# Performance work log

Measured on AMD Instinct MI355X. Metric: run time of the kernel, lower is better.

The kernel has to match this reference:

```python
import jax, jax.numpy as jnp
import numpy as np

B, N, C = 8, 1024, 1024
H = 16
D = C // H  # head_dim = 64
SCALE = D ** -0.5


def setup_inputs() -> dict:
    key = jax.random.key(0)
    k1, k2, k3 = jax.random.split(key, 3)
    x = jax.random.normal(k1, (B, N, C), dtype=jnp.float32)
    w_qkv = jax.random.normal(k2, (3 * C, C), dtype=jnp.float32) * (C ** -0.5)
    w_proj = jax.random.normal(k3, (C, C), dtype=jnp.float32) * (C ** -0.5)
    b_proj = jnp.zeros((C,), dtype=jnp.float32)
    return {"x": x, "w_qkv": w_qkv, "w_proj": w_proj, "b_proj": b_proj}


def reference(x, w_qkv, w_proj, b_proj):
    Bx, Nx, Cx = x.shape
    # qkv: [B,N,3C] -> [3,B,H,N,D]
    qkv = jnp.einsum('bnc,oc->bno', x, w_qkv)
    qkv = qkv.reshape(Bx, Nx, 3, H, D).transpose(2, 0, 3, 1, 4)
    q, k, v = qkv[0], qkv[1], qkv[2]
    attn = jnp.einsum('bhnd,bhmd->bhnm', q, k) * SCALE  # [B,H,N,N]
    attn = jax.nn.softmax(attn, axis=-1)
    out = jnp.einsum('bhnm,bhmd->bhnd', attn, v)  # [B,H,N,D]
    out = out.transpose(0, 2, 1, 3).reshape(Bx, Nx, Cx)
    return jnp.einsum('bnc,oc->bno', out, w_proj) + b_proj
```

## Files before the change

kernel.cpp:

```cpp
#include <hip/hip_runtime.h>

typedef _Float16 half8 __attribute__((ext_vector_type(8)));
typedef _Float16 half4v __attribute__((ext_vector_type(4)));
typedef _Float16 half2v __attribute__((ext_vector_type(2)));
typedef float floatx4 __attribute__((ext_vector_type(4)));

#define AS3 __attribute__((address_space(3)))
#define AS1 __attribute__((address_space(1)))

__global__ __launch_bounds__(256) void cvt_all(const float* __restrict__ x,
                                               const float* __restrict__ wq,
                                               const float* __restrict__ wp,
                                               _Float16* __restrict__ xh,
                                               _Float16* __restrict__ wqh,
                                               _Float16* __restrict__ wph) {
    long i = (long)blockIdx.x * 256 + threadIdx.x;
    const float4* src; half4v* dst; long off;
    if (i < 2097152)      { src = (const float4*)x;  dst = (half4v*)xh;  off = i; }
    else if (i < 2883584) { src = (const float4*)wq; dst = (half4v*)wqh; off = i - 2097152; }
    else                  { src = (const float4*)wp; dst = (half4v*)wph; off = i - 2883584; }
    float4 v = src[off];
    half4v h = {(_Float16)v.x, (_Float16)v.y, (_Float16)v.z, (_Float16)v.w};
    dst[off] = h;
}

__global__ __launch_bounds__(256, 4) void gemm_tn(
    const _Float16* __restrict__ A, const _Float16* __restrict__ B,
    _Float16* __restrict__ Ch, int ldc, _Float16* __restrict__ Vt, int split,
    float* __restrict__ Cf, const float* __restrict__ bias,
    int M, int Nn, int K)
{
    __shared__ _Float16 sA[2][128 * 32];
    __shared__ _Float16 sB[2][128 * 32];
    const int tid  = threadIdx.x;
    const int lane = tid & 63, wave = tid >> 6;
    const int quad = lane >> 4, l16 = lane & 15;
    const int wr = wave >> 1, wc = wave & 1;
    const long m0 = (long)blockIdx.x * 128, n0 = (long)blockIdx.y * 128;

    const int srow = tid >> 2;
    const int sslot = ((tid & 3) ^ ((srow >> 1) & 3)) * 8;
    const int dlo = srow * 32 + sslot;
    const int dhi = (srow + 64) * 32 + sslot;
    const _Float16* gA0 = A + (m0 + srow) * (long)K + (tid & 3) * 8;
    const _Float16* gA1 = A + (m0 + srow + 64) * (long)K + (tid & 3) * 8;
    const _Float16* gB0 = B + (n0 + srow) * (long)K + (tid & 3) * 8;
    const _Float16* gB1 = B + (n0 + srow + 64) * (long)K + (tid & 3) * 8;

    const int swz = (l16 >> 1) & 3;
    const int aoff = ((quad ^ swz) * 8);

    floatx4 acc[4][4] = {};
    const int nk = K >> 5;

    half8 rA0 = *(const half8*)gA0, rA1 = *(const half8*)gA1;
    half8 rB0 = *(const half8*)gB0, rB1 = *(const half8*)gB1;
    *(half8*)&sA[0][dlo] = rA0; *(half8*)&sA[0][dhi] = rA1;
    *(half8*)&sB[0][dlo] = rB0; *(half8*)&sB[0][dhi] = rB1;

    for (int kk = 0; kk < nk; kk++) {
        const int cur = kk & 1;
        __syncthreads();
        const bool more = (kk + 1 < nk);
        if (more) {
            const long k0 = (long)(kk + 1) << 5;
            rA0 = *(const half8*)(gA0 + k0); rA1 = *(const half8*)(gA1 + k0);
            rB0 = *(const half8*)(gB0 + k0); rB1 = *(const half8*)(gB1 + k0);
        }

        const _Float16* cA = &sA[cur][0];
        const _Float16* cB = &sB[cur][0];
        half8 af[4], bf[4];
#pragma unroll
        for (int t = 0; t < 4; t++)
            af[t] = *(const half8*)&cA[(wr * 64 + t * 16 + l16) * 32 + aoff];
#pragma unroll
        for (int t = 0; t < 4; t++)
            bf[t] = *(const half8*)&cB[(wc * 64 + t * 16 + l16) * 32 + aoff];
#pragma unroll
        for (int tm = 0; tm < 4; tm++)
#pragma unroll
            for (int tn = 0; tn < 4; tn++)
                acc[tm][tn] = __builtin_amdgcn_mfma_f32_16x16x32_f16(af[tm], bf[tn], acc[tm][tn], 0, 0, 0);

        if (more) {
            _Float16* nA = &sA[cur ^ 1][0];
            _Float16* nB = &sB[cur ^ 1][0];
            *(half8*)&nA[dlo] = rA0; *(half8*)&nA[dhi] = rA1;
            *(half8*)&nB[dlo] = rB0; *(half8*)&nB[dhi] = rB1;
        }
    }

#pragma unroll
    for (int tm = 0; tm < 4; tm++) {
        long row = m0 + wr * 64 + tm * 16 + quad * 4;
#pragma unroll
        for (int tn = 0; tn < 4; tn++) {
            long col = n0 + wc * 64 + tn * 16 + l16;
            if (Cf) {
                float bv = bias ? bias[col] : 0.f;
#pragma unroll
                for (int r = 0; r < 4; r++)
                    Cf[(row + r) * (long)Nn + col] = acc[tm][tn][r] + bv;
            } else if (col >= split) {
                long cv = col - split;
                long vrow = ((row >> 10) * 16 + (cv >> 6)) * 64 + (cv & 63);
                long nn = row & 1023;
                half4v pv = {(_Float16)acc[tm][tn][0], (_Float16)acc[tm][tn][1],
                             (_Float16)acc[tm][tn][2], (_Float16)acc[tm][tn][3]};
                *(half4v*)&Vt[vrow * 1024 + nn] = pv;
            } else {
#pragma unroll
                for (int r = 0; r < 4; r++)
                    Ch[(row + r) * (long)ldc + col] = (_Float16)acc[tm][tn][r];
            }
        }
    }
}

#define QSC 0.18033688f
__global__ __launch_bounds__(256, 3) void flash_attn(const _Float16* __restrict__ qk,
                                                     const _Float16* __restrict__ vt,
                                                     _Float16* __restrict__ out)
{
    const int bh = blockIdx.x, b = bh >> 4, h = bh & 15;
    const int n0 = blockIdx.y * 128;
    const int tid = threadIdx.x, lane = tid & 63, wave = tid >> 6;
    const int quad = lane >> 4, l16 = lane & 15;

    __shared__ _Float16 sK[64 * 72];
    __shared__ _Float16 sVT[64 * 72];
    __shared__ _Float16 sPT[4][32 * 72];

    half8 qf[2][2];
    const _Float16 qs = (_Float16)QSC;
    const _Float16* qbase = qk + (long)(b * 1024 + n0 + wave * 32) * 2048 + h * 64;
#pragma unroll
    for (int t = 0; t < 2; t++)
#pragma unroll
        for (int s = 0; s < 2; s++) {
            half8 v = *(const half8*)(qbase + (long)(t * 16 + l16) * 2048 + s * 32 + quad * 8);
#pragma unroll
            for (int j = 0; j < 8; j++) v[j] *= qs;
            qf[t][s] = v;
        }

    const int srow = tid >> 3, scol8 = (tid & 7) * 8;
    const _Float16* kgb = qk + 1024 + h * 64 + scol8 + (long)(b * 1024 + srow) * 2048;
    const _Float16* vgb = vt + (long)(bh * 64 + srow) * 1024 + scol8;

    float m_[2] = {-1e30f, -1e30f}, l_[2] = {0.f, 0.f};
    floatx4 o[2][4] = {};

    half8 kreg[2], vreg[2];
#pragma unroll
    for (int i = 0; i < 2; i++) {
        kreg[i] = *(const half8*)(kgb + (long)(i * 32) * 2048);
        vreg[i] = *(const half8*)(vgb + (long)(i * 32) * 1024);
    }

    for (int kt = 0; kt < 16; kt++) {
        __syncthreads();
#pragma unroll
        for (int i = 0; i < 2; i++) {
            *(half8*)&sK[(srow + i * 32) * 72 + scol8]  = kreg[i];
            *(half8*)&sVT[(srow + i * 32) * 72 + scol8] = vreg[i];
        }
        __syncthreads();
        if (kt + 1 < 16) {
            const int kr1 = (kt + 1) * 64;
#pragma unroll
            for (int i = 0; i < 2; i++) {
                kreg[i] = *(const half8*)(kgb + (long)(kr1 + i * 32) * 2048);
                vreg[i] = *(const half8*)(vgb + (long)(i * 32) * 1024 + kr1);
            }
        }

        floatx4 sacc[2][4] = {};
#pragma unroll
        for (int c = 0; c < 4; c++)
#pragma unroll
            for (int s = 0; s < 2; s++) {
                half8 kf = *(const half8*)&sK[(c * 16 + l16) * 72 + s * 32 + quad * 8];
                sacc[0][c] = __builtin_amdgcn_mfma_f32_16x16x32_f16(kf, qf[0][s], sacc[0][c], 0, 0, 0);
                sacc[1][c] = __builtin_amdgcn_mfma_f32_16x16x32_f16(kf, qf[1][s], sacc[1][c], 0, 0, 0);
            }

#pragma unroll
        for (int t = 0; t < 2; t++) {
            float mx = -1e30f;
#pragma unroll
            for (int c = 0; c < 4; c++)
#pragma unroll
                for (int r = 0; r < 4; r++) mx = fmaxf(mx, sacc[t][c][r]);
            mx = fmaxf(mx, __shfl_xor(mx, 16));
            mx = fmaxf(mx, __shfl_xor(mx, 32));
            float mn = fmaxf(m_[t], mx);
            float al = exp2f(m_[t] - mn);
            m_[t] = mn;
            float rs = 0.f;
#pragma unroll
            for (int c = 0; c < 4; c++)
#pragma unroll
                for (int r = 0; r < 4; r++) {
                    float p = exp2f(sacc[t][c][r] - mn);
                    sacc[t][c][r] = p;
                    rs += p;
                }
            rs += __shfl_xor(rs, 16);
            rs += __shfl_xor(rs, 32);
            l_[t] = l_[t] * al + rs;
#pragma unroll
            for (int dt = 0; dt < 4; dt++) o[t][dt] *= al;
#pragma unroll
            for (int c = 0; c < 4; c++) {
                half4v p = {(_Float16)sacc[t][c][0], (_Float16)sacc[t][c][1],
                            (_Float16)sacc[t][c][2], (_Float16)sacc[t][c][3]};
                *(half4v*)&sPT[wave][(t * 16 + l16) * 72 + c * 16 + quad * 4] = p;
            }
        }

#pragma unroll
        for (int kk = 0; kk < 2; kk++) {
            half8 pf0 = *(const half8*)&sPT[wave][(l16) * 72 + kk * 32 + quad * 8];
            half8 pf1 = *(const half8*)&sPT[wave][(16 + l16) * 72 + kk * 32 + quad * 8];
#pragma unroll
            for (int dt = 0; dt < 4; dt++) {
                half8 vf = *(const half8*)&sVT[(dt * 16 + l16) * 72 + kk * 32 + quad * 8];
                o[0][dt] = __builtin_amdgcn_mfma_f32_16x16x32_f16(vf, pf0, o[0][dt], 0, 0, 0);
                o[1][dt] = __builtin_amdgcn_mfma_f32_16x16x32_f16(vf, pf1, o[1][dt], 0, 0, 0);
            }
        }
    }

#pragma unroll
    for (int t = 0; t < 2; t++) {
        float inv = 1.f / l_[t];
#pragma unroll
        for (int dt = 0; dt < 4; dt++) {
            floatx4 v = o[t][dt];
            half4v a = {(_Float16)(v[0] * inv), (_Float16)(v[1] * inv),
                        (_Float16)(v[2] * inv), (_Float16)(v[3] * inv)};
            *(half4v*)&sPT[wave][(t * 16 + l16) * 72 + dt * 16 + quad * 4] = a;
        }
    }
    __syncthreads();
#pragma unroll
    for (int i = 0; i < 4; i++) {
        int ql = i * 8 + (lane >> 3);
        int c8 = (lane & 7) * 8;
        half8 vv = *(const half8*)&sPT[wave][ql * 72 + c8];
        *(half8*)(out + (long)(b * 1024 + n0 + wave * 32 + ql) * 1024 + h * 64 + c8) = vv;
    }
}

extern "C" void kernel_launch(void* const* d_in, const int* in_sizes, int n_in,
                              void* d_out, int out_size, void* d_ws, size_t ws_size,
                              hipStream_t stream) {
    const float* x      = (const float*)d_in[0];
    const float* w_qkv  = (const float*)d_in[1];
    const float* w_proj = (const float*)d_in[2];
    const float* b_proj = (const float*)d_in[3];

    char* ws = (char*)d_ws;
    _Float16* qkh    = (_Float16*)ws;
    _Float16* vT     = (_Float16*)(ws + 33554432);
    _Float16* xh     = (_Float16*)(ws + 50331648);
    _Float16* wqkvh  = (_Float16*)(ws + 67108864);
    _Float16* wprojh = (_Float16*)(ws + 73400320);
    _Float16* attnh  = xh;

    cvt_all<<<12288, 256, 0, stream>>>(x, w_qkv, w_proj, xh, wqkvh, wprojh);

    gemm_tn<<<dim3(64, 24), 256, 0, stream>>>(xh, wqkvh, qkh, 2048, vT, 2048,
                                              nullptr, nullptr, 8192, 3072, 1024);
    flash_attn<<<dim3(128, 8), 256, 0, stream>>>(qkh, vT, attnh);
    gemm_tn<<<dim3(64, 8), 256, 0, stream>>>(attnh, wprojh, nullptr, 0, nullptr, 1 << 30,
                                             (float*)d_out, b_proj, 8192, 1024, 1024);
}
```

Measured before the change: 261.9 us.

## Deepen GEMM global prefetch to two stages, drop attention register prefetch, retune occupancy

```diff
diff --git a/kernel.cpp b/kernel.cpp
--- a/kernel.cpp
+++ b/kernel.cpp
@@ -2,7 +2,6 @@
 
 typedef _Float16 half8 __attribute__((ext_vector_type(8)));
 typedef _Float16 half4v __attribute__((ext_vector_type(4)));
-typedef _Float16 half2v __attribute__((ext_vector_type(2)));
 typedef float floatx4 __attribute__((ext_vector_type(4)));
 
 #define AS3 __attribute__((address_space(3)))
@@ -24,7 +23,7 @@
     dst[off] = h;
 }
 
-__global__ __launch_bounds__(256, 4) void gemm_tn(
+__global__ __launch_bounds__(256, 3) void gemm_tn(
     const _Float16* __restrict__ A, const _Float16* __restrict__ B,
     _Float16* __restrict__ Ch, int ldc, _Float16* __restrict__ Vt, int split,
     float* __restrict__ Cf, const float* __restrict__ bias,
@@ -53,41 +52,52 @@
     floatx4 acc[4][4] = {};
     const int nk = K >> 5;
 
-    half8 rA0 = *(const half8*)gA0, rA1 = *(const half8*)gA1;
-    half8 rB0 = *(const half8*)gB0, rB1 = *(const half8*)gB1;
-    *(half8*)&sA[0][dlo] = rA0; *(half8*)&sA[0][dhi] = rA1;
-    *(half8*)&sB[0][dlo] = rB0; *(half8*)&sB[0][dhi] = rB1;
-
-    for (int kk = 0; kk < nk; kk++) {
-        const int cur = kk & 1;
-        __syncthreads();
-        const bool more = (kk + 1 < nk);
-        if (more) {
-            const long k0 = (long)(kk + 1) << 5;
-            rA0 = *(const half8*)(gA0 + k0); rA1 = *(const half8*)(gA1 + k0);
-            rB0 = *(const half8*)(gB0 + k0); rB1 = *(const half8*)(gB1 + k0);
-        }
-
-        const _Float16* cA = &sA[cur][0];
-        const _Float16* cB = &sB[cur][0];
-        half8 af[4], bf[4];
-#pragma unroll
-        for (int t = 0; t < 4; t++)
-            af[t] = *(const half8*)&cA[(wr * 64 + t * 16 + l16) * 32 + aoff];
-#pragma unroll
-        for (int t = 0; t < 4; t++)
-            bf[t] = *(const half8*)&cB[(wc * 64 + t * 16 + l16) * 32 + aoff];
-#pragma unroll
-        for (int tm = 0; tm < 4; tm++)
-#pragma unroll
-            for (int tn = 0; tn < 4; tn++)
-                acc[tm][tn] = __builtin_amdgcn_mfma_f32_16x16x32_f16(af[tm], bf[tn], acc[tm][tn], 0, 0, 0);
-
-        if (more) {
-            _Float16* nA = &sA[cur ^ 1][0];
-            _Float16* nB = &sB[cur ^ 1][0];
-            *(half8*)&nA[dlo] = rA0; *(half8*)&nA[dhi] = rA1;
-            *(half8*)&nB[dlo] = rB0; *(half8*)&nB[dhi] = rB1;
+    {
+        half8 a0 = *(const half8*)gA0, a1 = *(const half8*)gA1;
+        half8 b0 = *(const half8*)gB0, b1 = *(const half8*)gB1;
+        *(half8*)&sA[0][dlo] = a0; *(half8*)&sA[0][dhi] = a1;
+        *(half8*)&sB[0][dlo] = b0; *(half8*)&sB[0][dhi] = b1;
+    }
+    half8 pA0[2], pA1[2], pB0[2], pB1[2];
+    pA0[0] = *(const half8*)(gA0 + 32); pA1[0] = *(const half8*)(gA1 + 32);
+    pB0[0] = *(const half8*)(gB0 + 32); pB1[0] = *(const half8*)(gB1 + 32);
+
+    for (int kk = 0; kk < nk; kk += 2) {
+#pragma unroll
+        for (int u = 0; u < 2; u++) {
+            const int k = kk + u;
+            __syncthreads();
+            if (k + 2 < nk) {
+                const long ko = (long)(k + 2) << 5;
+                pA0[u ^ 1] = *(const half8*)(gA0 + ko);
+                pA1[u ^ 1] = *(const half8*)(gA1 + ko);
+                pB0[u ^ 1] = *(const half8*)(gB0 + ko);
+                pB1[u ^ 1] = *(const half8*)(gB1 + ko);
+            }
+
+            const _Float16* cA = &sA[u][0];
+            const _Float16* cB = &sB[u][0];
+            half8 af[4], bf[4];
+#pragma unroll
+            for (int t = 0; t < 4; t++)
+                af[t] = *(const half8*)&cA[(wr * 64 + t * 16 + l16) * 32 + aoff];
+#pragma unroll
+            for (int t = 0; t < 4; t++)
+                bf[t] = *(const half8*)&cB[(wc * 64 + t * 16 + l16) * 32 + aoff];
+#pragma unroll
+            for (int tm = 0; tm < 4; tm++)
+#pragma unroll
+                for (int tn = 0; tn < 4; tn++)
+                    acc[tm][tn] = __builtin_amdgcn_mfma_f32_16x16x32_f16(af[tm], bf[tn], acc[tm][tn], 0, 0, 0);
+
+            if (k + 1 < nk) {
+                _Float16* nA = &sA[u ^ 1][0];
+                _Float16* nB = &sB[u ^ 1][0];
+                *(half8*)&nA[dlo] = pA0[u];
+                *(half8*)&nA[dhi] = pA1[u];
+                *(half8*)&nB[dlo] = pB0[u];
+                *(half8*)&nB[dhi] = pB1[u];
+            }
         }
     }
 
@@ -119,7 +129,7 @@
 }
 
 #define QSC 0.18033688f
-__global__ __launch_bounds__(256, 3) void flash_attn(const _Float16* __restrict__ qk,
+__global__ __launch_bounds__(256, 4) void flash_attn(const _Float16* __restrict__ qk,
                                                      const _Float16* __restrict__ vt,
                                                      _Float16* __restrict__ out)
 {
@@ -152,29 +162,16 @@
     float m_[2] = {-1e30f, -1e30f}, l_[2] = {0.f, 0.f};
     floatx4 o[2][4] = {};
 
-    half8 kreg[2], vreg[2];
-#pragma unroll
-    for (int i = 0; i < 2; i++) {
-        kreg[i] = *(const half8*)(kgb + (long)(i * 32) * 2048);
-        vreg[i] = *(const half8*)(vgb + (long)(i * 32) * 1024);
-    }
-
     for (int kt = 0; kt < 16; kt++) {
+        const int kr0 = kt * 64;
         __syncthreads();
 #pragma unroll
         for (int i = 0; i < 2; i++) {
-            *(half8*)&sK[(srow + i * 32) * 72 + scol8]  = kreg[i];
-            *(half8*)&sVT[(srow + i * 32) * 72 + scol8] = vreg[i];
+            int r = srow + i * 32;
+            *(half8*)&sK[r * 72 + scol8]  = *(const half8*)(kgb + (long)(kr0 + i * 32) * 2048);
+            *(half8*)&sVT[r * 72 + scol8] = *(const half8*)(vgb + (long)(i * 32) * 1024 + kr0);
         }
         __syncthreads();
-        if (kt + 1 < 16) {
-            const int kr1 = (kt + 1) * 64;
-#pragma unroll
-            for (int i = 0; i < 2; i++) {
-                kreg[i] = *(const half8*)(kgb + (long)(kr1 + i * 32) * 2048);
-                vreg[i] = *(const half8*)(vgb + (long)(i * 32) * 1024 + kr1);
-            }
-        }
 
         floatx4 sacc[2][4] = {};
 #pragma unroll
```

After: 253.6 us. -3.2%, faster.
